# Optimization experiments

Measured on AMD Instinct MI355X. Metric: run time of the kernel, lower is better.

Reference implementation:

```python
import jax, jax.numpy as jnp
import numpy as np

TEMPERATURE = 0.2
EPS = 1e-12  # matches torch F.normalize eps


def _l2_normalize(x):
    n = jnp.linalg.norm(x, axis=-1, keepdims=True)
    return x / jnp.maximum(n, EPS)


def setup_inputs() -> dict:
    key = jax.random.key(0)
    k1, k2 = jax.random.split(key)
    B, D = 8192, 256
    return {
        "user_embeddings": jax.random.normal(k1, (B, D), dtype=jnp.float32),
        "positive_item_embeddings": jax.random.normal(k2, (B, D), dtype=jnp.float32),
    }


def reference(user_embeddings, positive_item_embeddings):
    # all_item_embeddings=None branch: in-batch implicit negatives.
    u = _l2_normalize(user_embeddings)            # [B, D]
    p = _l2_normalize(positive_item_embeddings)   # [B, D]
    sim = jnp.einsum("bd,nd->bn", u, p) / TEMPERATURE  # [B, B]
    pos_sim = jnp.diagonal(sim)                   # [B]; equals the torch pos_sim
    # Original concatenates pos_sim[i] with the off-diagonal row entries and takes
    # logsumexp. Since the diagonal of sim IS pos_sim[i], that set equals the full
    # row, so loss_i = -pos_sim_i + logsumexp(sim[i, :]). Vectorized over the batch.
    lse = jax.nn.logsumexp(sim, axis=1)           # [B]
    return jnp.mean(lse - pos_sim)
```

## Files before the change

### kernel.cpp

```cpp
#include <hip/hip_runtime.h>
#include <hip/hip_bf16.h>

#define DDIM 256
#define NROWS 8192

typedef __attribute__((ext_vector_type(8))) __bf16 bf16x8;
typedef __attribute__((ext_vector_type(4))) float floatx4;

__device__ __forceinline__ void async16(const void* g, void* l) {
    __builtin_amdgcn_global_load_lds(
        (const __attribute__((address_space(1))) unsigned int*)g,
        (__attribute__((address_space(3))) unsigned int*)l,
        16, 0, 0);
}

__device__ __forceinline__ void stage_rows(const unsigned short* __restrict__ g,
                                           unsigned short* l,
                                           int wv, int lane,
                                           int rows_per_wave, int ninstr)
{
    const int lrow = lane >> 5;
    const int gcol = lane & 31;
    const int r0 = wv * rows_per_wave;
    for (int j = 0; j < ninstr; ++j) {
        const int rb = r0 + j * 2;
        const int r  = rb + lrow;
        const int gg = gcol ^ (r & 7);
        async16(g + (size_t)r * DDIM + gg * 8, l + (size_t)rb * DDIM);
    }
}

__device__ __forceinline__ bf16x8 frag(const unsigned short* base, int row,
                                       int ks, int q, int m)
{
    return *(const bf16x8*)&base[(size_t)row * DDIM
                                 + (((ks * 4 + q) ^ (m & 7)) * 8)];
}

__global__ __launch_bounds__(256) void normalize_kernel(
    const float* __restrict__ U, const float* __restrict__ P,
    unsigned short* __restrict__ Un, unsigned short* __restrict__ Pn,
    float* __restrict__ possim, float* __restrict__ rowsum,
    float* __restrict__ out, int* __restrict__ counter)
{
    if (blockIdx.x == 0 && threadIdx.x == 0) { out[0] = 0.0f; counter[0] = 0; }
    const int lane = threadIdx.x & 63;
    const int row  = blockIdx.x * 4 + (threadIdx.x >> 6);
    const size_t base = (size_t)row * DDIM + lane * 4;
    const float4 u4 = *(const float4*)(U + base);
    const float4 p4 = *(const float4*)(P + base);
    float su = u4.x*u4.x + u4.y*u4.y + u4.z*u4.z + u4.w*u4.w;
    float sp = p4.x*p4.x + p4.y*p4.y + p4.z*p4.z + p4.w*p4.w;
    float up = u4.x*p4.x + u4.y*p4.y + u4.z*p4.z + u4.w*p4.w;
    #pragma unroll
    for (int d = 1; d < 64; d <<= 1) {
        su += __shfl_xor(su, d);
        sp += __shfl_xor(sp, d);
        up += __shfl_xor(up, d);
    }
    const float iu = rsqrtf(fmaxf(su, 1e-24f));
    const float ip = rsqrtf(fmaxf(sp, 1e-24f));
    if (lane == 0) {
        possim[row] = up * iu * ip;
        rowsum[row] = 0.0f;
    }
    union { ushort4 s4; __hip_bfloat16 h[4]; } cu, cp;
    cu.h[0] = __float2bfloat16(u4.x * iu); cu.h[1] = __float2bfloat16(u4.y * iu);
    cu.h[2] = __float2bfloat16(u4.z * iu); cu.h[3] = __float2bfloat16(u4.w * iu);
    cp.h[0] = __float2bfloat16(p4.x * ip); cp.h[1] = __float2bfloat16(p4.y * ip);
    cp.h[2] = __float2bfloat16(p4.z * ip); cp.h[3] = __float2bfloat16(p4.w * ip);
    *(ushort4*)(Un + base) = cu.s4;
    *(ushort4*)(Pn + base) = cp.s4;
}

__global__ __launch_bounds__(256, 2) void sim_exp_rowsum(
    const unsigned short* __restrict__ Un,
    const unsigned short* __restrict__ Pn,
    float* __restrict__ rowsum,
    const float* __restrict__ possim,
    int* __restrict__ counter,
    float* __restrict__ out)
{
    __shared__ __align__(16) unsigned short lds[32768];
    __shared__ float ws4[4];
    __shared__ int ticket_s;

    const int tid  = threadIdx.x;
    const int lane = tid & 63;
    const int wv   = tid >> 6;
    const int wr   = wv >> 1, wc = wv & 1;
    const int m = lane & 15;
    const int q = lane >> 4;

    const int stripe = blockIdx.x >> 3;
    const int oct    = blockIdx.x & 7;

    const unsigned short* Aglob = Un + (size_t)stripe * 128 * DDIM;
    stage_rows(Aglob, lds, wv, lane, 32, 16);
    __syncthreads();

    bf16x8 afr[4][8];
    #pragma unroll
    for (int t = 0; t < 4; ++t)
        #pragma unroll
        for (int ks = 0; ks < 8; ++ks)
            afr[t][ks] = frag(lds, wr * 64 + t * 16 + m, ks, q, m);
    __syncthreads();

    const unsigned short* Bglob = Pn + (size_t)(oct * 1024) * DDIM;
    float rowpart[4][4];
    #pragma unroll
    for (int t = 0; t < 4; ++t)
        #pragma unroll
        for (int r = 0; r < 4; ++r)
            rowpart[t][r] = 0.0f;

    stage_rows(Bglob, lds, wv, lane, 16, 8);

    for (int i = 0; i < 16; ++i) {
        __syncthreads();
        if (i < 15)
            stage_rows(Bglob + (size_t)(i + 1) * 64 * DDIM,
                       lds + ((i + 1) & 1) * 16384, wv, lane, 16, 8);
        const unsigned short* Bp = lds + (i & 1) * 16384;

        floatx4 acc[4][2];
        #pragma unroll
        for (int t = 0; t < 4; ++t) {
            acc[t][0] = {0.0f, 0.0f, 0.0f, 0.0f};
            acc[t][1] = {0.0f, 0.0f, 0.0f, 0.0f};
        }
        #pragma unroll
        for (int ks = 0; ks < 8; ++ks) {
            const bf16x8 b0 = frag(Bp, wc * 32 + m,      ks, q, m);
            const bf16x8 b1 = frag(Bp, wc * 32 + 16 + m, ks, q, m);
            #pragma unroll
            for (int t = 0; t < 4; ++t) {
                acc[t][0] = __builtin_amdgcn_mfma_f32_16x16x32_bf16(
                    afr[t][ks], b0, acc[t][0], 0, 0, 0);
                acc[t][1] = __builtin_amdgcn_mfma_f32_16x16x32_bf16(
                    afr[t][ks], b1, acc[t][1], 0, 0, 0);
            }
        }
        #pragma unroll
        for (int t = 0; t < 4; ++t)
            #pragma unroll
            for (int r = 0; r < 4; ++r)
                rowpart[t][r] += __expf(5.0f * acc[t][0][r])
                               + __expf(5.0f * acc[t][1][r]);
    }

    #pragma unroll
    for (int t = 0; t < 4; ++t) {
        #pragma unroll
        for (int r = 0; r < 4; ++r) {
            float s = rowpart[t][r];
            s += __shfl_xor(s, 1);
            s += __shfl_xor(s, 2);
            s += __shfl_xor(s, 4);
            s += __shfl_xor(s, 8);
            if (m == 0) {
                const int grow = stripe * 128 + wr * 64 + t * 16 + q * 4 + r;
                atomicAdd(&rowsum[grow], s);
            }
        }
    }

    __threadfence();
    __syncthreads();
    if (tid == 0)
        ticket_s = __hip_atomic_fetch_add(counter, 1, __ATOMIC_ACQ_REL,
                                          __HIP_MEMORY_SCOPE_AGENT);
    __syncthreads();
    if (ticket_s == 511) {
        float part = 0.0f;
        for (int i = tid; i < NROWS; i += 256) {
            const float rs = __hip_atomic_load(&rowsum[i], __ATOMIC_RELAXED,
                                               __HIP_MEMORY_SCOPE_AGENT);
            part += __logf(rs) - 5.0f * possim[i];
        }
        #pragma unroll
        for (int d = 1; d < 64; d <<= 1) part += __shfl_xor(part, d);
        if (lane == 0) ws4[wv] = part;
        __syncthreads();
        if (tid == 0)
            out[0] = (ws4[0] + ws4[1] + ws4[2] + ws4[3]) * (1.0f / (float)NROWS);
    }
}

extern "C" void kernel_launch(void* const* d_in, const int* in_sizes, int n_in,
                              void* d_out, int out_size, void* d_ws, size_t ws_size,
                              hipStream_t stream) {
    const float* U = (const float*)d_in[0];
    const float* P = (const float*)d_in[1];
    float* out = (float*)d_out;
    char* ws = (char*)d_ws;
    unsigned short* Un = (unsigned short*)ws;
    unsigned short* Pn = (unsigned short*)(ws + 4194304);
    float* rowsum = (float*)(ws + 8388608);
    float* possim = (float*)(ws + 8388608 + 32768);
    int* counter  = (int*)(ws + 8388608 + 65536);

    normalize_kernel<<<NROWS / 4, 256, 0, stream>>>(U, P, Un, Pn, possim, rowsum,
                                                    out, counter);
    sim_exp_rowsum<<<512, 256, 0, stream>>>(Un, Pn, rowsum, possim, counter, out);
}
```

Before: 144.6 us.

## Pre-pack normalized embeddings into MFMA fragment order and load directly from global

The normalize kernel now writes the bf16 embeddings in MFMA fragment order, staging them through shared memory so that each lane's 16-byte fragment is contiguous in global memory. The GEMM kernel drops its LDS staging, double buffering and barriers and reads its A and B fragments straight from global or L2 with coalesced vector loads. This removes LDS traffic and synchronisation but loses the explicit prefetch overlap, so global load latency is now exposed inside the MFMA loop. The exponential is also rewritten as exp2 with a folded constant.

```diff
diff --git a/kernel.cpp b/kernel.cpp
--- a/kernel.cpp
+++ b/kernel.cpp
@@ -3,111 +3,103 @@
 
 #define DDIM 256
 #define NROWS 8192
+#define LOG2E5 7.2134752044448170f
 
 typedef __attribute__((ext_vector_type(8))) __bf16 bf16x8;
 typedef __attribute__((ext_vector_type(4))) float floatx4;
 
-__device__ __forceinline__ void async16(const void* g, void* l) {
-    __builtin_amdgcn_global_load_lds(
-        (const __attribute__((address_space(1))) unsigned int*)g,
-        (__attribute__((address_space(3))) unsigned int*)l,
-        16, 0, 0);
-}
 
-__device__ __forceinline__ void stage_rows(const unsigned short* __restrict__ g,
-                                           unsigned short* l,
-                                           int wv, int lane,
-                                           int rows_per_wave, int ninstr)
-{
-    const int lrow = lane >> 5;
-    const int gcol = lane & 31;
-    const int r0 = wv * rows_per_wave;
-    for (int j = 0; j < ninstr; ++j) {
-        const int rb = r0 + j * 2;
-        const int r  = rb + lrow;
-        const int gg = gcol ^ (r & 7);
-        async16(g + (size_t)r * DDIM + gg * 8, l + (size_t)rb * DDIM);
-    }
-}
-
-__device__ __forceinline__ bf16x8 frag(const unsigned short* base, int row,
-                                       int ks, int q, int m)
-{
-    return *(const bf16x8*)&base[(size_t)row * DDIM
-                                 + (((ks * 4 + q) ^ (m & 7)) * 8)];
-}
-
-__global__ __launch_bounds__(256) void normalize_kernel(
+__global__ __launch_bounds__(256) void normalize_repack(
     const float* __restrict__ U, const float* __restrict__ P,
-    unsigned short* __restrict__ Un, unsigned short* __restrict__ Pn,
+    unsigned short* __restrict__ Af, unsigned short* __restrict__ Pf,
     float* __restrict__ possim, float* __restrict__ rowsum,
     float* __restrict__ out, int* __restrict__ counter)
 {
-    if (blockIdx.x == 0 && threadIdx.x == 0) { out[0] = 0.0f; counter[0] = 0; }
-    const int lane = threadIdx.x & 63;
-    const int row  = blockIdx.x * 4 + (threadIdx.x >> 6);
-    const size_t base = (size_t)row * DDIM + lane * 4;
-    const float4 u4 = *(const float4*)(U + base);
-    const float4 p4 = *(const float4*)(P + base);
-    float su = u4.x*u4.x + u4.y*u4.y + u4.z*u4.z + u4.w*u4.w;
-    float sp = p4.x*p4.x + p4.y*p4.y + p4.z*p4.z + p4.w*p4.w;
-    float up = u4.x*p4.x + u4.y*p4.y + u4.z*p4.z + u4.w*p4.w;
+    __shared__ unsigned short Ut[16 * 264];
+    __shared__ unsigned short Pt[16 * 264];
+    const int tid = threadIdx.x;
+    const int R   = blockIdx.x;
+    const int r16 = tid >> 4;
+    const int c   = tid & 15;
+    const int row = R * 16 + r16;
+
+    if (R == 0 && tid == 0) { out[0] = 0.0f; counter[0] = 0; }
+    if (c == 0) rowsum[row] = 0.0f;
+
+    float4 u4[4], p4[4];
+    float su = 0.0f, sp = 0.0f, up = 0.0f;
     #pragma unroll
-    for (int d = 1; d < 64; d <<= 1) {
+    for (int j = 0; j < 4; ++j) {
+        const size_t base = (size_t)row * DDIM + c * 16 + j * 4;
+        u4[j] = *(const float4*)(U + base);
+        p4[j] = *(const float4*)(P + base);
+        su += u4[j].x*u4[j].x + u4[j].y*u4[j].y + u4[j].z*u4[j].z + u4[j].w*u4[j].w;
+        sp += p4[j].x*p4[j].x + p4[j].y*p4[j].y + p4[j].z*p4[j].z + p4[j].w*p4[j].w;
+        up += u4[j].x*p4[j].x + u4[j].y*p4[j].y + u4[j].z*p4[j].z + u4[j].w*p4[j].w;
+    }
+    #pragma unroll
+    for (int d = 1; d < 16; d <<= 1) {
         su += __shfl_xor(su, d);
         sp += __shfl_xor(sp, d);
         up += __shfl_xor(up, d);
     }
     const float iu = rsqrtf(fmaxf(su, 1e-24f));
     const float ip = rsqrtf(fmaxf(sp, 1e-24f));
-    if (lane == 0) {
-        possim[row] = up * iu * ip;
-        rowsum[row] = 0.0f;
+    if (c == 0) possim[row] = up * iu * ip;
+
+    #pragma unroll
+    for (int j = 0; j < 4; ++j) {
+        union { ushort4 s4; __hip_bfloat16 h[4]; } cu, cp;
+        cu.h[0] = __float2bfloat16(u4[j].x * iu); cu.h[1] = __float2bfloat16(u4[j].y * iu);
+        cu.h[2] = __float2bfloat16(u4[j].z * iu); cu.h[3] = __float2bfloat16(u4[j].w * iu);
+        cp.h[0] = __float2bfloat16(p4[j].x * ip); cp.h[1] = __float2bfloat16(p4[j].y * ip);
+        cp.h[2] = __float2bfloat16(p4[j].z * ip); cp.h[3] = __float2bfloat16(p4[j].w * ip);
+        *(ushort4*)&Ut[r16 * 264 + c * 16 + j * 4] = cu.s4;
+        *(ushort4*)&Pt[r16 * 264 + c * 16 + j * 4] = cp.s4;
     }
-    union { ushort4 s4; __hip_bfloat16 h[4]; } cu, cp;
-    cu.h[0] = __float2bfloat16(u4.x * iu); cu.h[1] = __float2bfloat16(u4.y * iu);
-    cu.h[2] = __float2bfloat16(u4.z * iu); cu.h[3] = __float2bfloat16(u4.w * iu);
-    cp.h[0] = __float2bfloat16(p4.x * ip); cp.h[1] = __float2bfloat16(p4.y * ip);
-    cp.h[2] = __float2bfloat16(p4.z * ip); cp.h[3] = __float2bfloat16(p4.w * ip);
-    *(ushort4*)(Un + base) = cu.s4;
-    *(ushort4*)(Pn + base) = cp.s4;
+    __syncthreads();
+
+    const int lane = tid & 63;
+    const int wv   = tid >> 6;
+    const int m = lane & 15, q = lane >> 4;
+    #pragma unroll
+    for (int g = 0; g < 2; ++g) {
+        const int G = wv * 2 + g;
+        const bf16x8 ua = *(const bf16x8*)&Ut[m * 264 + G * 32 + q * 8];
+        const bf16x8 pa = *(const bf16x8*)&Pt[m * 264 + G * 32 + q * 8];
+        const size_t o = ((size_t)(R * 8 + G) * 64 + lane) * 8;
+        *(bf16x8*)(Af + o) = ua;
+        *(bf16x8*)(Pf + o) = pa;
+    }
 }
 
 __global__ __launch_bounds__(256, 2) void sim_exp_rowsum(
-    const unsigned short* __restrict__ Un,
-    const unsigned short* __restrict__ Pn,
+    const unsigned short* __restrict__ Af,
+    const unsigned short* __restrict__ Pf,
     float* __restrict__ rowsum,
     const float* __restrict__ possim,
     int* __restrict__ counter,
     float* __restrict__ out)
 {
-    __shared__ __align__(16) unsigned short lds[32768];
     __shared__ float ws4[4];
     __shared__ int ticket_s;
-
     const int tid  = threadIdx.x;
     const int lane = tid & 63;
     const int wv   = tid >> 6;
     const int wr   = wv >> 1, wc = wv & 1;
-    const int m = lane & 15;
-    const int q = lane >> 4;
+    const int m = lane & 15, q = lane >> 4;
 
+    const int oct    = blockIdx.x & 7;
     const int stripe = blockIdx.x >> 3;
-    const int oct    = blockIdx.x & 7;
-
-    const unsigned short* Aglob = Un + (size_t)stripe * 128 * DDIM;
-    stage_rows(Aglob, lds, wv, lane, 32, 16);
-    __syncthreads();
 
     bf16x8 afr[4][8];
     #pragma unroll
     for (int t = 0; t < 4; ++t)
         #pragma unroll
         for (int ks = 0; ks < 8; ++ks)
-            afr[t][ks] = frag(lds, wr * 64 + t * 16 + m, ks, q, m);
-    __syncthreads();
+            afr[t][ks] = *(const bf16x8*)(Af +
+                ((size_t)((stripe * 8 + wr * 4 + t) * 8 + ks) * 64 + lane) * 8);
 
-    const unsigned short* Bglob = Pn + (size_t)(oct * 1024) * DDIM;
     float rowpart[4][4];
     #pragma unroll
     for (int t = 0; t < 4; ++t)
@@ -115,14 +107,9 @@
         for (int r = 0; r < 4; ++r)
             rowpart[t][r] = 0.0f;
 
-    stage_rows(Bglob, lds, wv, lane, 16, 8);
-
     for (int i = 0; i < 16; ++i) {
-        __syncthreads();
-        if (i < 15)
-            stage_rows(Bglob + (size_t)(i + 1) * 64 * DDIM,
-                       lds + ((i + 1) & 1) * 16384, wv, lane, 16, 8);
-        const unsigned short* Bp = lds + (i & 1) * 16384;
+        const int RB0 = oct * 64 + i * 4 + wc * 2;
+        const unsigned short* B0 = Pf + ((size_t)RB0 * 8 * 64 + lane) * 8;
 
         floatx4 acc[4][2];
         #pragma unroll
@@ -132,8 +119,8 @@
         }
         #pragma unroll
         for (int ks = 0; ks < 8; ++ks) {
-            const bf16x8 b0 = frag(Bp, wc * 32 + m,      ks, q, m);
-            const bf16x8 b1 = frag(Bp, wc * 32 + 16 + m, ks, q, m);
+            const bf16x8 b0 = *(const bf16x8*)(B0 + (size_t)ks * 512);
+            const bf16x8 b1 = *(const bf16x8*)(B0 + (size_t)(8 + ks) * 512);
             #pragma unroll
             for (int t = 0; t < 4; ++t) {
                 acc[t][0] = __builtin_amdgcn_mfma_f32_16x16x32_bf16(
@@ -146,8 +133,8 @@
         for (int t = 0; t < 4; ++t)
             #pragma unroll
             for (int r = 0; r < 4; ++r)
-                rowpart[t][r] += __expf(5.0f * acc[t][0][r])
-                               + __expf(5.0f * acc[t][1][r]);
+                rowpart[t][r] += exp2f(LOG2E5 * acc[t][0][r])
+                               + exp2f(LOG2E5 * acc[t][1][r]);
     }
 
     #pragma unroll
@@ -174,10 +161,10 @@
     __syncthreads();
     if (ticket_s == 511) {
         float part = 0.0f;
-        for (int i = tid; i < NROWS; i += 256) {
-            const float rs = __hip_atomic_load(&rowsum[i], __ATOMIC_RELAXED,
+        for (int idx = tid; idx < NROWS; idx += 256) {
+            const float rs = __hip_atomic_load(&rowsum[idx], __ATOMIC_RELAXED,
                                                __HIP_MEMORY_SCOPE_AGENT);
-            part += __logf(rs) - 5.0f * possim[i];
+            part += __logf(rs) - 5.0f * possim[idx];
         }
         #pragma unroll
         for (int d = 1; d < 64; d <<= 1) part += __shfl_xor(part, d);
@@ -195,13 +182,13 @@
     const float* P = (const float*)d_in[1];
     float* out = (float*)d_out;
     char* ws = (char*)d_ws;
-    unsigned short* Un = (unsigned short*)ws;
-    unsigned short* Pn = (unsigned short*)(ws + 4194304);
+    unsigned short* Af = (unsigned short*)ws;
+    unsigned short* Pf = (unsigned short*)(ws + 4194304);
     float* rowsum = (float*)(ws + 8388608);
     float* possim = (float*)(ws + 8388608 + 32768);
     int* counter  = (int*)(ws + 8388608 + 65536);
 
-    normalize_kernel<<<NROWS / 4, 256, 0, stream>>>(U, P, Un, Pn, possim, rowsum,
-                                                    out, counter);
-    sim_exp_rowsum<<<512, 256, 0, stream>>>(Un, Pn, rowsum, possim, counter, out);
+    normalize_repack<<<NROWS / 16, 256, 0, stream>>>(U, P, Af, Pf, possim, rowsum,
+                                                     out, counter);
+    sim_exp_rowsum<<<512, 256, 0, stream>>>(Af, Pf, rowsum, possim, counter, out);
 }
```

Result: slower. 156.1 us (+8.0%).

## Quantize normalized embeddings to FP8 and use FP8 MFMA with smaller row tiles

Applied to the files above, without the earlier changes.

Normalization now writes FP8 (packed via cvt_pk_fp8) in place of bf16, halving the operand bytes. The similarity GEMM switches to the 16x16x32 fp8 MFMA. Each block now covers 64 user rows instead of 128, so the grid grows to 1024 blocks with occupancy hint 3. exp is computed via exp2f with a folded constant. FP8 lowers similarity precision, which could perturb the logsumexp result beyond tolerance, and the smaller A tile reduces reuse of each staged B tile.

```diff
diff --git a/kernel.cpp b/kernel.cpp
--- a/kernel.cpp
+++ b/kernel.cpp
@@ -1,10 +1,11 @@
 #include <hip/hip_runtime.h>
 #include <hip/hip_bf16.h>
+#include <stdint.h>
 
 #define DDIM 256
 #define NROWS 8192
-
-typedef __attribute__((ext_vector_type(8))) __bf16 bf16x8;
+#define LOG2E5 7.2134752044448170f
+
 typedef __attribute__((ext_vector_type(4))) float floatx4;
 
 __device__ __forceinline__ void async16(const void* g, void* l) {
@@ -14,32 +15,9 @@
         16, 0, 0);
 }
 
-__device__ __forceinline__ void stage_rows(const unsigned short* __restrict__ g,
-                                           unsigned short* l,
-                                           int wv, int lane,
-                                           int rows_per_wave, int ninstr)
-{
-    const int lrow = lane >> 5;
-    const int gcol = lane & 31;
-    const int r0 = wv * rows_per_wave;
-    for (int j = 0; j < ninstr; ++j) {
-        const int rb = r0 + j * 2;
-        const int r  = rb + lrow;
-        const int gg = gcol ^ (r & 7);
-        async16(g + (size_t)r * DDIM + gg * 8, l + (size_t)rb * DDIM);
-    }
-}
-
-__device__ __forceinline__ bf16x8 frag(const unsigned short* base, int row,
-                                       int ks, int q, int m)
-{
-    return *(const bf16x8*)&base[(size_t)row * DDIM
-                                 + (((ks * 4 + q) ^ (m & 7)) * 8)];
-}
-
-__global__ __launch_bounds__(256) void normalize_kernel(
+__global__ __launch_bounds__(256) void normalize_fp8(
     const float* __restrict__ U, const float* __restrict__ P,
-    unsigned short* __restrict__ Un, unsigned short* __restrict__ Pn,
+    unsigned char* __restrict__ Uq, unsigned char* __restrict__ Pq,
     float* __restrict__ possim, float* __restrict__ rowsum,
     float* __restrict__ out, int* __restrict__ counter)
 {
@@ -64,24 +42,24 @@
         possim[row] = up * iu * ip;
         rowsum[row] = 0.0f;
     }
-    union { ushort4 s4; __hip_bfloat16 h[4]; } cu, cp;
-    cu.h[0] = __float2bfloat16(u4.x * iu); cu.h[1] = __float2bfloat16(u4.y * iu);
-    cu.h[2] = __float2bfloat16(u4.z * iu); cu.h[3] = __float2bfloat16(u4.w * iu);
-    cp.h[0] = __float2bfloat16(p4.x * ip); cp.h[1] = __float2bfloat16(p4.y * ip);
-    cp.h[2] = __float2bfloat16(p4.z * ip); cp.h[3] = __float2bfloat16(p4.w * ip);
-    *(ushort4*)(Un + base) = cu.s4;
-    *(ushort4*)(Pn + base) = cp.s4;
-}
-
-__global__ __launch_bounds__(256, 2) void sim_exp_rowsum(
-    const unsigned short* __restrict__ Un,
-    const unsigned short* __restrict__ Pn,
+    int pu = __builtin_amdgcn_cvt_pk_fp8_f32(u4.x * iu, u4.y * iu, 0, false);
+    pu     = __builtin_amdgcn_cvt_pk_fp8_f32(u4.z * iu, u4.w * iu, pu, true);
+    int pp = __builtin_amdgcn_cvt_pk_fp8_f32(p4.x * ip, p4.y * ip, 0, false);
+    pp     = __builtin_amdgcn_cvt_pk_fp8_f32(p4.z * ip, p4.w * ip, pp, true);
+    ((int*)Uq)[(size_t)row * 64 + lane] = pu;
+    ((int*)Pq)[(size_t)row * 64 + lane] = pp;
+}
+
+__global__ __launch_bounds__(256, 3) void sim_exp_rowsum(
+    const unsigned char* __restrict__ Uq,
+    const unsigned char* __restrict__ Pq,
     float* __restrict__ rowsum,
     const float* __restrict__ possim,
     int* __restrict__ counter,
     float* __restrict__ out)
 {
-    __shared__ __align__(16) unsigned short lds[32768];
+    __shared__ __align__(16) unsigned char As[64 * 256];
+    __shared__ __align__(16) unsigned char Bs[2][64 * 256];
     __shared__ float ws4[4];
     __shared__ int ticket_s;
 
@@ -89,69 +67,96 @@
     const int lane = tid & 63;
     const int wv   = tid >> 6;
     const int wr   = wv >> 1, wc = wv & 1;
-    const int m = lane & 15;
-    const int q = lane >> 4;
-
+    const int m = lane & 15, q = lane >> 4;
+
+    const int oct    = blockIdx.x & 7;
     const int stripe = blockIdx.x >> 3;
-    const int oct    = blockIdx.x & 7;
-
-    const unsigned short* Aglob = Un + (size_t)stripe * 128 * DDIM;
-    stage_rows(Aglob, lds, wv, lane, 32, 16);
+
+    const int r_off = lane >> 4;
+    const int Pg    = lane & 15;
+
+    const unsigned char* Ag = Uq + (size_t)stripe * 64 * DDIM;
+    const unsigned char* Bg = Pq + (size_t)oct * 1024 * DDIM;
+
+    #pragma unroll
+    for (int j = 0; j < 4; ++j) {
+        const int r0 = wv * 16 + j * 4;
+        const int r  = r0 + r_off;
+        async16(Ag + (size_t)r * DDIM + ((Pg ^ (r & 7)) * 16), &As[r0 * 256]);
+    }
+    #pragma unroll
+    for (int j = 0; j < 4; ++j) {
+        const int r0 = wv * 16 + j * 4;
+        const int r  = r0 + r_off;
+        async16(Bg + (size_t)r * DDIM + ((Pg ^ (r & 7)) * 16), &Bs[0][r0 * 256]);
+    }
     __syncthreads();
 
-    bf16x8 afr[4][8];
-    #pragma unroll
-    for (int t = 0; t < 4; ++t)
-        #pragma unroll
-        for (int ks = 0; ks < 8; ++ks)
-            afr[t][ks] = frag(lds, wr * 64 + t * 16 + m, ks, q, m);
-    __syncthreads();
-
-    const unsigned short* Bglob = Pn + (size_t)(oct * 1024) * DDIM;
-    float rowpart[4][4];
-    #pragma unroll
-    for (int t = 0; t < 4; ++t)
+    int64_t afr[2][8];
+    #pragma unroll
+    for (int t = 0; t < 2; ++t) {
+        const int arow = wr * 32 + t * 16 + m;
+        #pragma unroll
+        for (int ks = 0; ks < 8; ++ks) {
+            const int G = 2 * ks + (q >> 1);
+            afr[t][ks] = *(const int64_t*)&As[arow * 256
+                             + ((G ^ (m & 7)) * 16) + (q & 1) * 8];
+        }
+    }
+
+    float rowpart[2][4];
+    #pragma unroll
+    for (int t = 0; t < 2; ++t)
         #pragma unroll
         for (int r = 0; r < 4; ++r)
             rowpart[t][r] = 0.0f;
 
-    stage_rows(Bglob, lds, wv, lane, 16, 8);
-
     for (int i = 0; i < 16; ++i) {
-        __syncthreads();
-        if (i < 15)
-            stage_rows(Bglob + (size_t)(i + 1) * 64 * DDIM,
-                       lds + ((i + 1) & 1) * 16384, wv, lane, 16, 8);
-        const unsigned short* Bp = lds + (i & 1) * 16384;
-
-        floatx4 acc[4][2];
-        #pragma unroll
-        for (int t = 0; t < 4; ++t) {
+        if (i > 0) __syncthreads();
+        if (i < 15) {
+            const unsigned char* Bt = Bg + (size_t)(i + 1) * 64 * DDIM;
+            unsigned char* dst = Bs[(i + 1) & 1];
+            #pragma unroll
+            for (int j = 0; j < 4; ++j) {
+                const int r0 = wv * 16 + j * 4;
+                const int r  = r0 + r_off;
+                async16(Bt + (size_t)r * DDIM + ((Pg ^ (r & 7)) * 16),
+                        dst + r0 * 256);
+            }
+        }
+        const unsigned char* Bp = Bs[i & 1];
+
+        floatx4 acc[2][2];
+        #pragma unroll
+        for (int t = 0; t < 2; ++t) {
             acc[t][0] = {0.0f, 0.0f, 0.0f, 0.0f};
             acc[t][1] = {0.0f, 0.0f, 0.0f, 0.0f};
         }
         #pragma unroll
         for (int ks = 0; ks < 8; ++ks) {
-            const bf16x8 b0 = frag(Bp, wc * 32 + m,      ks, q, m);
-            const bf16x8 b1 = frag(Bp, wc * 32 + 16 + m, ks, q, m);
+            const int G = 2 * ks + (q >> 1);
+            const int gofs = ((G ^ (m & 7)) * 16) + (q & 1) * 8;
+            const int brow0 = wc * 32 + m;
+            const int64_t b0 = *(const int64_t*)&Bp[brow0 * 256 + gofs];
+            const int64_t b1 = *(const int64_t*)&Bp[(brow0 + 16) * 256 + gofs];
             #pragma unroll
-            for (int t = 0; t < 4; ++t) {
-                acc[t][0] = __builtin_amdgcn_mfma_f32_16x16x32_bf16(
+            for (int t = 0; t < 2; ++t) {
+                acc[t][0] = __builtin_amdgcn_mfma_f32_16x16x32_fp8_fp8(
                     afr[t][ks], b0, acc[t][0], 0, 0, 0);
-                acc[t][1] = __builtin_amdgcn_mfma_f32_16x16x32_bf16(
+                acc[t][1] = __builtin_amdgcn_mfma_f32_16x16x32_fp8_fp8(
                     afr[t][ks], b1, acc[t][1], 0, 0, 0);
             }
         }
         #pragma unroll
-        for (int t = 0; t < 4; ++t)
+        for (int t = 0; t < 2; ++t)
             #pragma unroll
             for (int r = 0; r < 4; ++r)
-                rowpart[t][r] += __expf(5.0f * acc[t][0][r])
-                               + __expf(5.0f * acc[t][1][r]);
-    }
-
-    #pragma unroll
-    for (int t = 0; t < 4; ++t) {
+                rowpart[t][r] += exp2f(LOG2E5 * acc[t][0][r])
+                               + exp2f(LOG2E5 * acc[t][1][r]);
+    }
+
+    #pragma unroll
+    for (int t = 0; t < 2; ++t) {
         #pragma unroll
         for (int r = 0; r < 4; ++r) {
             float s = rowpart[t][r];
@@ -160,7 +165,7 @@
             s += __shfl_xor(s, 4);
             s += __shfl_xor(s, 8);
             if (m == 0) {
-                const int grow = stripe * 128 + wr * 64 + t * 16 + q * 4 + r;
+                const int grow = stripe * 64 + wr * 32 + t * 16 + q * 4 + r;
                 atomicAdd(&rowsum[grow], s);
             }
         }
@@ -172,12 +177,12 @@
         ticket_s = __hip_atomic_fetch_add(counter, 1, __ATOMIC_ACQ_REL,
                                           __HIP_MEMORY_SCOPE_AGENT);
     __syncthreads();
-    if (ticket_s == 511) {
+    if (ticket_s == 1023) {
         float part = 0.0f;
-        for (int i = tid; i < NROWS; i += 256) {
-            const float rs = __hip_atomic_load(&rowsum[i], __ATOMIC_RELAXED,
+        for (int idx = tid; idx < NROWS; idx += 256) {
+            const float rs = __hip_atomic_load(&rowsum[idx], __ATOMIC_RELAXED,
                                                __HIP_MEMORY_SCOPE_AGENT);
-            part += __logf(rs) - 5.0f * possim[i];
+            part += __logf(rs) - 5.0f * possim[idx];
         }
         #pragma unroll
         for (int d = 1; d < 64; d <<= 1) part += __shfl_xor(part, d);
@@ -195,13 +200,13 @@
     const float* P = (const float*)d_in[1];
     float* out = (float*)d_out;
     char* ws = (char*)d_ws;
-    unsigned short* Un = (unsigned short*)ws;
-    unsigned short* Pn = (unsigned short*)(ws + 4194304);
-    float* rowsum = (float*)(ws + 8388608);
-    float* possim = (float*)(ws + 8388608 + 32768);
-    int* counter  = (int*)(ws + 8388608 + 65536);
-
-    normalize_kernel<<<NROWS / 4, 256, 0, stream>>>(U, P, Un, Pn, possim, rowsum,
-                                                    out, counter);
-    sim_exp_rowsum<<<512, 256, 0, stream>>>(Un, Pn, rowsum, possim, counter, out);
-}
+    unsigned char* Uq = (unsigned char*)ws;
+    unsigned char* Pq = (unsigned char*)(ws + 2097152);
+    float* rowsum = (float*)(ws + 4194304);
+    float* possim = (float*)(ws + 4194304 + 32768);
+    int* counter  = (int*)(ws + 4194304 + 65536);
+
+    normalize_fp8<<<NROWS / 4, 256, 0, stream>>>(U, P, Uq, Pq, possim, rowsum,
+                                                 out, counter);
+    sim_exp_rowsum<<<1024, 256, 0, stream>>>(Uq, Pq, rowsum, possim, counter, out);
+}
```

Measured after the change: 187.3 us. 1.3x slower.
